# Kernel tuning notes

Measured on AMD Instinct MI355X. Metric: run time of the kernel, lower is better.

## Reference

```python
import jax, jax.numpy as jnp
import numpy as np

S, B, V, E, H = 64, 32, 32000, 512, 1024


def gru_cell(x, h, Wih, Whh, bih, bhh):
    # PyTorch GRU cell math. x: [B, in], h: [B, H]
    gi = x @ Wih.T + bih          # [B, 3H]
    gh = h @ Whh.T + bhh          # [B, 3H]
    ir, iz, inn = jnp.split(gi, 3, axis=-1)
    hr, hz, hn = jnp.split(gh, 3, axis=-1)
    r = jax.nn.sigmoid(ir + hr)
    z = jax.nn.sigmoid(iz + hz)
    n = jnp.tanh(inn + r * hn)
    return (1.0 - z) * n + z * h


def run_gru(xs, h0, Wih, Whh, bih, bhh):
    def step(h, x):
        h = gru_cell(x, h, Wih, Whh, bih, bhh)
        return h, h
    _, hs = jax.lax.scan(step, h0, xs)
    return hs  # [S, B, H]


def setup_inputs():
    key = jax.random.key(0)
    ks = jax.random.split(key, 24)
    n = lambda k, shp, s=0.05: (jax.random.normal(k, shp, jnp.float32) * s)
    inp = {
        "input_seq": jax.random.randint(ks[0], (S, B), 0, V),
        "target_seq": jax.random.randint(ks[1], (S, B), 0, V),
        "emb": n(ks[2], (V, E)),
        # bidirectional encoder GRU (forward / backward directions)
        "enc_Wih_f": n(ks[3], (3 * H, E)), "enc_Whh_f": n(ks[4], (3 * H, H)),
        "enc_bih_f": n(ks[5], (3 * H,)),  "enc_bhh_f": n(ks[6], (3 * H,)),
        "enc_Wih_b": n(ks[7], (3 * H, E)), "enc_Whh_b": n(ks[8], (3 * H, H)),
        "enc_bih_b": n(ks[9], (3 * H,)),  "enc_bhh_b": n(ks[10], (3 * H,)),
        "encoder_init": n(ks[11], (2, H), 0.1),
        # decoder GRU: input = token(E) + glimpse(2H) + last_output(E)
        "dec_Wih": n(ks[12], (3 * H, 2 * E + 2 * H)), "dec_Whh": n(ks[13], (3 * H, H)),
        "dec_bih": n(ks[14], (3 * H,)), "dec_bhh": n(ks[15], (3 * H,)),
        "dec_init_h": n(ks[16], (H,), 0.1),
        "dec_init_out": n(ks[17], (E,), 0.1),
        "attn_W1": n(ks[18], (H, 3 * H)),  # Linear(3H -> H, bias=False)
        "attn_W2": n(ks[19], (1, H)),      # Linear(H -> 1, bias=False)
        "out_W": n(ks[20], (V, H)), "out_b": n(ks[21], (V,)),
    }
    return inp


def reference(input_seq, target_seq, emb,
              enc_Wih_f, enc_Whh_f, enc_bih_f, enc_bhh_f,
              enc_Wih_b, enc_Whh_b, enc_bih_b, enc_bhh_b, encoder_init,
              dec_Wih, dec_Whh, dec_bih, dec_bhh, dec_init_h, dec_init_out,
              attn_W1, attn_W2, out_W, out_b):
    x = emb[input_seq]            # [S, B, E]
    tgt = emb[target_seq]         # [S, B, E]
    bsz = x.shape[1]

    # bidirectional encoder
    h0f = jnp.broadcast_to(encoder_init[0], (bsz, H))
    h0b = jnp.broadcast_to(encoder_init[1], (bsz, H))
    fwd = run_gru(x, h0f, enc_Wih_f, enc_Whh_f, enc_bih_f, enc_bhh_f)
    bwd = run_gru(x[::-1], h0b, enc_Wih_b, enc_Whh_b, enc_bih_b, enc_bhh_b)[::-1]
    enc = jnp.concatenate([fwd, bwd], axis=-1)  # [S, B, 2H]

    def step(carry, inp_t):
        h, last_out = carry                      # [B,H], [B,E]
        tok, tg = inp_t                          # [B,E], [B,E]
        hexp = jnp.broadcast_to(h[None], (S, bsz, H))
        a = jnp.concatenate([enc, hexp], axis=-1)            # [S, B, 3H]
        scores = jnp.tanh(a @ attn_W1.T) @ attn_W2.T          # [S, B, 1]
        # NOTE: original uses nn.Softmax(dim=1) on [S,B,1] -> softmax over BATCH dim
        w = jax.nn.softmax(scores, axis=1)
        glimpse = (enc * w).sum(axis=0)                       # [B, 2H]
        dec_in = jnp.concatenate([tok, glimpse, last_out], axis=-1)
        h = gru_cell(dec_in, h, dec_Wih, dec_Whh, dec_bih, dec_bhh)
        probs = jax.nn.softmax(h @ out_W.T + out_b, axis=1)   # [B, V]
        return (h, tg), probs

    h0 = jnp.broadcast_to(dec_init_h, (bsz, H))
    o0 = jnp.broadcast_to(dec_init_out, (bsz, E))
    _, outs = jax.lax.scan(step, (h0, o0), (x, tgt))
    return outs  # [S, B, V]
```

## Files before the change

kernel.cpp:

```cpp
#include <hip/hip_runtime.h>
#include <hip/hip_bf16.h>

#define S_ 64
#define B_ 32
#define V_ 32000
#define E_ 512
#define H_ 1024
#define H3_ 3072

typedef __hip_bfloat16 bf16;
typedef __attribute__((ext_vector_type(8))) short s8v;
typedef __attribute__((ext_vector_type(4))) float f4;
typedef unsigned long long ull;

__device__ __forceinline__ float b2f(bf16 x){ return __bfloat162float(x); }
__device__ __forceinline__ bf16  f2b(float x){ return __float2bfloat16(x); }
__device__ __forceinline__ float bfu2f(unsigned short u){
  union { unsigned u; float f; } c; c.u = ((unsigned)u) << 16; return c.f;
}
#define MFMA16(a,b,c) __builtin_amdgcn_mfma_f32_16x16x32_bf16((a),(b),(c),0,0,0)

__device__ __forceinline__ float fsigmoid(float x){ return 1.f/(1.f + __expf(-x)); }
__device__ __forceinline__ float ftanh(float x){ float e2 = __expf(2.f*x); return 1.f - 2.f/(e2 + 1.f); }

__device__ __forceinline__ void gl16(const bf16* g, bf16* l){
  __builtin_amdgcn_global_load_lds((const __attribute__((address_space(1))) void*)g,
                                   (__attribute__((address_space(3))) void*)l, 16, 0, 0);
}

__device__ __forceinline__ ull dld64(const void* p){
  return __hip_atomic_load((const ull*)p, __ATOMIC_RELAXED, __HIP_MEMORY_SCOPE_AGENT);
}
__device__ __forceinline__ void dst64(void* p, ull v){
  __hip_atomic_store((ull*)p, v, __ATOMIC_RELAXED, __HIP_MEMORY_SCOPE_AGENT);
}
__device__ __forceinline__ float dldf(const void* p){
  unsigned u = __hip_atomic_load((const unsigned*)p, __ATOMIC_RELAXED, __HIP_MEMORY_SCOPE_AGENT);
  union{unsigned u; float f;} c; c.u=u; return c.f;
}
__device__ __forceinline__ unsigned dldu(const unsigned* p){
  return __hip_atomic_load(p, __ATOMIC_RELAXED, __HIP_MEMORY_SCOPE_AGENT);
}
__device__ __forceinline__ void dstu(unsigned* p, unsigned v){
  __hip_atomic_store(p, v, __ATOMIC_RELAXED, __HIP_MEMORY_SCOPE_AGENT);
}

__device__ __forceinline__ void pbar(unsigned* bar, unsigned ep, int bid, int nblk){
  __syncthreads();
  if (bid == 0){
    const int i = threadIdx.x;
    if (i > 0 && i < nblk){
      while (dldu(bar + i*32) < ep) __builtin_amdgcn_s_sleep(1);
    }
    __syncthreads();
    if (i < nblk) dstu(bar + 4096 + i*32, ep);
  } else if (threadIdx.x == 0){
    dstu(bar + bid*32, ep);
    while (dldu(bar + 4096 + bid*32) < ep) __builtin_amdgcn_s_sleep(1);
  }
  __syncthreads();
  asm volatile("" ::: "memory");
}

__device__ __forceinline__ void cast8(const float* __restrict__ s, bf16* __restrict__ d, int i){
  f4 a = *((const f4*)s + (size_t)i*2);
  f4 b = *((const f4*)s + (size_t)i*2 + 1);
  union { s8v v; bf16 h[8]; } o;
  #pragma unroll
  for (int k=0;k<4;k++){ o.h[k]=f2b(a[k]); o.h[4+k]=f2b(b[k]); }
  *((s8v*)d + i) = o.v;
}

__global__ __launch_bounds__(256) void prep_all_k(
  const float* __restrict__ emb, const int* __restrict__ iseq, const int* __restrict__ tseq,
  const float* __restrict__ dino,
  const float* __restrict__ wihf, const float* __restrict__ wihb,
  const float* __restrict__ whhf, const float* __restrict__ whhb,
  const float* __restrict__ whhd, const float* __restrict__ w1,
  const float* __restrict__ wihd, const float* __restrict__ outw,
  const float* __restrict__ einit, const float* __restrict__ bihf,
  const float* __restrict__ bihb, const float* __restrict__ dinh,
  bf16* __restrict__ x_b, bf16* __restrict__ lo_b,
  bf16* __restrict__ wihf_b, bf16* __restrict__ wihb_b,
  bf16* __restrict__ whhf_b, bf16* __restrict__ whhb_b,
  bf16* __restrict__ whhd_b, bf16* __restrict__ w1_b,
  bf16* __restrict__ wihd_b, bf16* __restrict__ outw_b,
  bf16* __restrict__ henc_b, float* __restrict__ hfE, float* __restrict__ bias_fb)
{
  const int task = blockIdx.y;
  const int stride = gridDim.x*256;
  const int i00 = blockIdx.x*256 + threadIdx.x;
  if (task < 8){
    const float* s; bf16* d; int n8;
    switch(task){
      case 0: s=wihf; d=wihf_b; n8=196608; break;
      case 1: s=wihb; d=wihb_b; n8=196608; break;
      case 2: s=whhf; d=whhf_b; n8=393216; break;
      case 3: s=whhb; d=whhb_b; n8=393216; break;
      case 4: s=whhd; d=whhd_b; n8=393216; break;
      case 5: s=w1;   d=w1_b;   n8=393216; break;
      case 6: s=wihd; d=wihd_b; n8=1179648; break;
      default: s=outw; d=outw_b; n8=4096000; break;
    }
    for (int i = i00; i < n8; i += stride) cast8(s, d, i);
  } else if (task == 8 || task == 9){
    for (int i = i00; i < 131072; i += stride){
      int row = i>>6, e8 = i&63;
      const float* src; bf16* d;
      if (task == 8){ src = emb + (size_t)iseq[row]*E_; d = x_b; }
      else {
        int t = row>>5, b = row&31;
        src = (t == 0) ? dino : (emb + (size_t)tseq[(t-1)*B_ + b]*E_);
        d = lo_b;
      }
      f4 a = *((const f4*)src + e8*2);
      f4 b = *((const f4*)src + e8*2 + 1);
      union { s8v v; bf16 h[8]; } o;
      #pragma unroll
      for (int k=0;k<4;k++){ o.h[k]=f2b(a[k]); o.h[4+k]=f2b(b[k]); }
      *((s8v*)d + i) = o.v;
    }
  } else {
    for (int i = i00; i < 8192; i += stride){
      int base = i*8;
      int dir = base>>15, rem = base&32767, col = rem&1023;
      const float* sp = einit + dir*H_ + col;
      f4 a = *(const f4*)sp, b = *(const f4*)(sp+4);
      union { s8v v; bf16 h[8]; } o;
      #pragma unroll
      for (int k=0;k<4;k++){ o.h[k]=f2b(a[k]); o.h[4+k]=f2b(b[k]); }
      *(s8v*)(henc_b + dir*32768 + rem) = o.v;
      *(f4*)(hfE + dir*32768 + rem) = a;
      *(f4*)(hfE + dir*32768 + rem + 4) = b;
      if (i < 6144) bias_fb[i] = (i < 3072) ? bihf[i] : bihb[i-3072];
    }
  }
}

template<int WB16>
__global__ __launch_bounds__(256) void gemm_bt(const bf16* __restrict__ A, int lda,
                                               const bf16* __restrict__ B, int ldb,
                                               const float* __restrict__ bias,
                                               void* __restrict__ Cp, int ldc, int K)
{
  __shared__ bf16 a_sm[128][32];
  __shared__ bf16 b_sm[128][32];
  const int tid = threadIdx.x;
  const int m0 = blockIdx.y*128, n0 = blockIdx.x*128;
  const int w = tid>>6, l = tid&63;
  const int wm = w>>1, wn = w&1;
  f4 acc[4][4];
  #pragma unroll
  for (int i=0;i<4;i++)
    #pragma unroll
    for (int j=0;j<4;j++) acc[i][j] = (f4){0.f,0.f,0.f,0.f};
  const int ar = l&15, koff = (l>>4)*8;
  const int glr = l>>2, gls = (l&3)*8;
  for (int k0 = 0; k0 < K; k0 += 32){
    __syncthreads();
    #pragma unroll
    for (int o = 0; o < 2; ++o){
      const int oo = w*2 + o;
      gl16(A + (size_t)(m0 + oo*16 + glr)*lda + k0 + gls, &a_sm[oo*16][0]);
      gl16(B + (size_t)(n0 + oo*16 + glr)*ldb + k0 + gls, &b_sm[oo*16][0]);
    }
    __syncthreads();
    s8v av[4], bv[4];
    #pragma unroll
    for (int i=0;i<4;i++) av[i] = *(const s8v*)&a_sm[wm*64 + i*16 + ar][koff];
    #pragma unroll
    for (int j=0;j<4;j++) bv[j] = *(const s8v*)&b_sm[wn*64 + j*16 + ar][koff];
    #pragma unroll
    for (int i=0;i<4;i++)
      #pragma unroll
      for (int j=0;j<4;j++)
        acc[i][j] = MFMA16(av[i], bv[j], acc[i][j]);
  }
  const int rb = (l>>4)*4;
  #pragma unroll
  for (int i=0;i<4;i++){
    #pragma unroll
    for (int j=0;j<4;j++){
      int col = n0 + wn*64 + j*16 + ar;
      float badd = bias ? bias[col] : 0.f;
      #pragma unroll
      for (int r=0;r<4;r++){
        int row = m0 + wm*64 + i*16 + rb + r;
        size_t idx = (size_t)row*ldc + col;
        float v = acc[i][j][r] + badd;
        if (WB16) ((bf16*)Cp)[idx] = f2b(v);
        else      ((float*)Cp)[idx] = v;
      }
    }
  }
}

__global__ __launch_bounds__(256) void gemm_dual(const bf16* __restrict__ A1, const bf16* __restrict__ A2,
                                                 const bf16* __restrict__ Bw, const float* __restrict__ bias,
                                                 float* __restrict__ C)
{
  __shared__ bf16 a_sm[128][32];
  __shared__ bf16 b_sm[128][32];
  const int tid = threadIdx.x;
  const int m0 = blockIdx.y*128, n0 = blockIdx.x*128;
  const int w = tid>>6, l = tid&63;
  const int wm = w>>1, wn = w&1;
  f4 acc[4][4];
  #pragma unroll
  for (int i=0;i<4;i++)
    #pragma unroll
    for (int j=0;j<4;j++) acc[i][j] = (f4){0.f,0.f,0.f,0.f};
  const int ar = l&15, koff = (l>>4)*8;
  const int glr = l>>2, gls = (l&3)*8;
  #pragma unroll 1
  for (int p = 0; p < 2; ++p){
    const bf16* Ax = p ? A2 : A1;
    const int cb = p ? 2560 : 0;
    for (int k0 = 0; k0 < 512; k0 += 32){
      __syncthreads();
      #pragma unroll
      for (int o = 0; o < 2; ++o){
        const int oo = w*2 + o;
        gl16(Ax + (size_t)(m0 + oo*16 + glr)*512 + k0 + gls, &a_sm[oo*16][0]);
        gl16(Bw + (size_t)(n0 + oo*16 + glr)*3072 + cb + k0 + gls, &b_sm[oo*16][0]);
      }
      __syncthreads();
      s8v av[4], bv[4];
      #pragma unroll
      for (int i=0;i<4;i++) av[i] = *(const s8v*)&a_sm[wm*64 + i*16 + ar][koff];
      #pragma unroll
      for (int j=0;j<4;j++) bv[j] = *(const s8v*)&b_sm[wn*64 + j*16 + ar][koff];
      #pragma unroll
      for (int i=0;i<4;i++)
        #pragma unroll
        for (int j=0;j<4;j++)
          acc[i][j] = MFMA16(av[i], bv[j], acc[i][j]);
    }
  }
  const int rb = (l>>4)*4;
  #pragma unroll
  for (int i=0;i<4;i++){
    #pragma unroll
    for (int j=0;j<4;j++){
      int col = n0 + wn*64 + j*16 + ar;
      float badd = bias[col];
      #pragma unroll
      for (int r=0;r<4;r++){
        int row = m0 + wm*64 + i*16 + rb + r;
        C[(size_t)row*H3_ + col] = acc[i][j][r] + badd;
      }
    }
  }
}

__global__ __launch_bounds__(256) void out_gemm_k(
  const bf16* __restrict__ A, const bf16* __restrict__ Bw,
  const float* __restrict__ bias, bf16* __restrict__ C)
{
  __shared__ bf16 a_sm[128][32];
  __shared__ bf16 b_sm[128][32];
  const int tid = threadIdx.x;
  const int bid = blockIdx.x;
  const int xcd = bid & 7, kk = bid >> 3;
  const int super = kk >> 6, rem = kk & 63;
  const int sm = super & 1, sn = super >> 1;
  const int mi = rem & 7, nj = rem >> 3;
  const int mt = sm*8 + mi, nl = sn*8 + nj;
  const int nt = nl*8 + xcd;
  if (nt >= 250) return;
  const int m0 = mt*128, n0 = nt*128;
  const int w = tid>>6, l = tid&63;
  const int wm = w>>1, wn = w&1;
  f4 acc[4][4];
  #pragma unroll
  for (int i=0;i<4;i++)
    #pragma unroll
    for (int j=0;j<4;j++) acc[i][j] = (f4){0.f,0.f,0.f,0.f};
  const int ar = l&15, koff = (l>>4)*8;
  const int glr = l>>2, gls = (l&3)*8;
  for (int k0 = 0; k0 < 1024; k0 += 32){
    __syncthreads();
    #pragma unroll
    for (int o = 0; o < 2; ++o){
      const int oo = w*2 + o;
      gl16(A + (size_t)(m0 + oo*16 + glr)*1024 + k0 + gls, &a_sm[oo*16][0]);
      gl16(Bw + (size_t)(n0 + oo*16 + glr)*1024 + k0 + gls, &b_sm[oo*16][0]);
    }
    __syncthreads();
    s8v av[4], bv[4];
    #pragma unroll
    for (int i=0;i<4;i++) av[i] = *(const s8v*)&a_sm[wm*64 + i*16 + ar][koff];
    #pragma unroll
    for (int j=0;j<4;j++) bv[j] = *(const s8v*)&b_sm[wn*64 + j*16 + ar][koff];
    #pragma unroll
    for (int i=0;i<4;i++)
      #pragma unroll
      for (int j=0;j<4;j++)
        acc[i][j] = MFMA16(av[i], bv[j], acc[i][j]);
  }
  const int rb = (l>>4)*4;
  float bj[4];
  #pragma unroll
  for (int j=0;j<4;j++) bj[j] = bias[n0 + wn*64 + j*16 + ar];
  #pragma unroll
  for (int i=0;i<4;i++){
    #pragma unroll
    for (int j=0;j<4;j++){
      const int col = n0 + wn*64 + j*16 + ar;
      #pragma unroll
      for (int r=0;r<4;r++){
        const int row = m0 + wm*64 + i*16 + rb + r;
        C[(size_t)row*V_ + col] = f2b(acc[i][j][r] + bj[j]);
      }
    }
  }
}

__global__ __launch_bounds__(256) void logit_stats_k(const bf16* __restrict__ lg,
                                                     float* __restrict__ rowM, float* __restrict__ rowL){
  __shared__ float wm[4], wl[4];
  const int tid = threadIdx.x;
  const bf16* p = lg + (size_t)blockIdx.x*V_;
  float m = -1e30f, lsum = 0.f;
  for (int c = tid; c < V_/8; c += 256){
    union { s8v v; unsigned short us[8]; } u;
    u.v = *((const s8v*)p + c);
    #pragma unroll
    for (int k = 0; k < 8; ++k){
      float v = bfu2f(u.us[k]);
      float mn = fmaxf(m, v);
      lsum = lsum*__expf(m - mn) + __expf(v - mn);
      m = mn;
    }
  }
  #pragma unroll
  for (int o = 32; o; o >>= 1){
    float mo = __shfl_xor(m, o), lo_ = __shfl_xor(lsum, o);
    float mn = fmaxf(m, mo);
    lsum = lsum*__expf(m - mn) + lo_*__expf(mo - mn);
    m = mn;
  }
  if ((tid&63)==0){ wm[tid>>6] = m; wl[tid>>6] = lsum; }
  __syncthreads();
  if (tid == 0){
    float M = fmaxf(fmaxf(wm[0],wm[1]), fmaxf(wm[2],wm[3]));
    float L = wl[0]*__expf(wm[0]-M) + wl[1]*__expf(wm[1]-M)
            + wl[2]*__expf(wm[2]-M) + wl[3]*__expf(wm[3]-M);
    rowM[blockIdx.x] = M;
    rowL[blockIdx.x] = L;
  }
}

__global__ __launch_bounds__(256) void norm_k(const bf16* __restrict__ lg,
                                              const float* __restrict__ rowM, const float* __restrict__ rowL,
                                              float* __restrict__ out){
  const int tid = threadIdx.x;
  const int row = blockIdx.x;
  const float M = rowM[row], inv = 1.f/rowL[row];
  const bf16* p = lg + (size_t)row*V_;
  float* q = out + (size_t)row*V_;
  for (int c = tid; c < V_/8; c += 256){
    union { s8v v; unsigned short us[8]; } u;
    u.v = *((const s8v*)p + c);
    f4 o0, o1;
    #pragma unroll
    for (int k = 0; k < 4; ++k) o0[k] = __expf(bfu2f(u.us[k]) - M)*inv;
    #pragma unroll
    for (int k = 0; k < 4; ++k) o1[k] = __expf(bfu2f(u.us[4+k]) - M)*inv;
    *((f4*)q + c*2)     = o0;
    *((f4*)q + c*2 + 1) = o1;
  }
}

__global__ __launch_bounds__(256) void enc_step_k(
  const float* __restrict__ gi_fb,
  const bf16* __restrict__ whhf, const bf16* __restrict__ whhb,
  const float* __restrict__ bhhf, const float* __restrict__ bhhb,
  const bf16* __restrict__ hrd_base, bf16* __restrict__ hwr_base,
  float* __restrict__ hfE, bf16* __restrict__ enc_out, int s)
{
  __shared__ bf16 hst[16][1032];
  __shared__ bf16 hsT[16][64];
  const int tid = threadIdx.x, bid = blockIdx.x;
  const int w = tid>>6, l = tid&63;
  const int lr = l&15, koff = (l>>4)*8, rb = (l>>4)*4;
  const int x = bid&7, g3 = bid>>3;
  const int dir = x>>2;
  const int mt = g3>>2;
  const int jtb = (x&3)*16 + (g3&3)*4;
  const int jt = jtb + w;
  const int col = jt*16 + lr;
  const bf16* W    = dir ? whhb : whhf;
  const float* bhh = dir ? bhhb : bhhf;
  const float br_ = bhh[col], bz_ = bhh[H_+col], bn_ = bhh[2*H_+col];
  const bf16* pr = W + (size_t)(jt*16 + lr)*H_ + koff;
  const bf16* pz = pr + (size_t)H_*H_;
  const bf16* pn = pz + (size_t)H_*H_;
  {
    const bf16* src = hrd_base + dir*32768 + (size_t)mt*16*H_;
    #pragma unroll
    for (int c = 0; c < 8; ++c){
      int g = c*256 + tid;
      int row = g>>7, off = g&127;
      *(s8v*)&hst[row][off*8] = *(const s8v*)(src + (size_t)row*H_ + off*8);
    }
  }
  __syncthreads();
  f4 accr = (f4){0,0,0,0}, accz = (f4){0,0,0,0}, accn = (f4){0,0,0,0};
  #pragma unroll 4
  for (int k0 = 0; k0 < H_; k0 += 32){
    s8v a = *(const s8v*)&hst[lr][koff + k0];
    accr = MFMA16(a, *(const s8v*)(pr + k0), accr);
    accz = MFMA16(a, *(const s8v*)(pz + k0), accz);
    accn = MFMA16(a, *(const s8v*)(pn + k0), accn);
  }
  const int es = dir ? (63 - s) : s;
  const int dcol = dir*3072 + col;
  #pragma unroll
  for (int ri = 0; ri < 4; ++ri){
    const int b_ = mt*16 + rb + ri;
    const size_t gr = (size_t)(es*B_ + b_)*6144;
    float ir = gi_fb[gr + dcol], iz = gi_fb[gr + 1024 + dcol], inn = gi_fb[gr + 2048 + dcol];
    float rg = fsigmoid(ir + accr[ri] + br_);
    float zg = fsigmoid(iz + accz[ri] + bz_);
    float ng = ftanh(inn + rg*(accn[ri] + bn_));
    float hold = hfE[dir*32768 + b_*H_ + col];
    float hnew = (1.f - zg)*ng + zg*hold;
    hfE[dir*32768 + b_*H_ + col] = hnew;
    hsT[rb+ri][w*16+lr] = f2b(hnew);
  }
  __syncthreads();
  {
    const int row = tid>>4, seg = tid&15;
    ull v = *(ull*)&hsT[row][seg*4];
    *(ull*)(hwr_base + dir*32768 + (size_t)(mt*16+row)*H_ + jtb*16 + seg*4) = v;
    *(ull*)(enc_out + (size_t)(es*B_ + mt*16+row)*2048 + dir*H_ + jtb*16 + seg*4) = v;
  }
}

__global__ __launch_bounds__(256) void dec_persist_k(
  const float* __restrict__ gi_d,
  const bf16* __restrict__ encW1b,
  const bf16* __restrict__ encWgb,
  const bf16* __restrict__ whhd, const float* __restrict__ bhhd,
  const bf16* __restrict__ w1b,
  const float* __restrict__ attnW2,
  const float* __restrict__ dinh,
  bf16* __restrict__ hdb,
  bf16* __restrict__ hW1b,
  float* __restrict__ gh,
  float* __restrict__ wat,
  bf16* __restrict__ h_all,
  unsigned* __restrict__ bar)
{
  __shared__ bf16 hst[16][1032];
  __shared__ float ghT[16][128];
  __shared__ bf16 hwT[16][128];
  __shared__ float w2st[1024];
  __shared__ float scl[32];
  __shared__ float watv[32];
  __shared__ float watst[64];
  __shared__ float part_[4][3][256];
  __shared__ bf16 hnewst[256];
  const int tid = threadIdx.x, bid = blockIdx.x;
  const int w = tid>>6, l = tid&63;
  const int lr = l&15, koff = (l>>4)*8;
  const int x = bid&7, g3 = bid>>3;
  const int db = 4*x + (g3&3), jq = g3>>2;
  const int jD = jq*256 + tid;
  w2st[tid] = attnW2[tid];
  w2st[tid+256] = attnW2[tid+256];
  w2st[tid+512] = attnW2[tid+512];
  w2st[tid+768] = attnW2[tid+768];
  float hreg = dinh[jD];
  hnewst[tid] = f2b(hreg);
  __syncthreads();
  if (tid < 64) dst64(hdb + (size_t)db*H_ + jq*256 + tid*4, *(ull*)&hnewst[tid*4]);
  pbar(bar, 1u, bid, 128);
  unsigned ep = 2u;
  for (int t = 0; t < 64; ++t){
    if (bid < 64){
      const bool isP = bid < 16;
      const int hmt = isP ? (bid&1) : ((bid-16)&1);
      {
        const bf16* src = hdb + (size_t)hmt*16*H_;
        #pragma unroll
        for (int c = 0; c < 16; ++c){
          int g = c*256 + tid;
          *(ull*)&hst[g>>8][(g&255)*4] = dld64(src + g*4);
        }
      }
      __syncthreads();
      if (isP){
        const int x2 = bid>>1;
        const int pjt0 = x2*8 + w*2;
        #pragma unroll
        for (int q = 0; q < 2; ++q){
          const bf16* pb = w1b + (size_t)((pjt0+q)*16 + lr)*H3_ + 2048 + koff;
          f4 acc = (f4){0,0,0,0};
          #pragma unroll 4
          for (int k0 = 0; k0 < H_; k0 += 32)
            acc = MFMA16(*(const s8v*)&hst[lr][koff+k0], *(const s8v*)(pb+k0), acc);
          #pragma unroll
          for (int r = 0; r < 4; ++r)
            hwT[(l>>4)*4+r][(w*2+q)*16 + lr] = f2b(acc[r]);
        }
        __syncthreads();
        #pragma unroll
        for (int i = 0; i < 2; ++i){
          int idx = tid + i*256;
          int row = idx>>5, seg = idx&31;
          dst64(hW1b + (size_t)(hmt*16+row)*H_ + x2*128 + seg*4, *(ull*)&hwT[row][seg*4]);
        }
      } else {
        const int gb = bid - 16;
        const int rest = gb>>1;
        const int x3 = rest/3, gkk = rest%3;
        const int ntb = x3*24 + gkk*8;
        #pragma unroll
        for (int q = 0; q < 2; ++q){
          const int nt = ntb + w*2 + q;
          const bf16* pb = whhd + (size_t)(nt*16 + lr)*H_ + koff;
          const float bv = bhhd[nt*16 + lr];
          f4 acc = (f4){0,0,0,0};
          #pragma unroll 4
          for (int k0 = 0; k0 < H_; k0 += 32)
            acc = MFMA16(*(const s8v*)&hst[lr][koff+k0], *(const s8v*)(pb+k0), acc);
          #pragma unroll
          for (int r = 0; r < 4; ++r)
            ghT[(l>>4)*4+r][(w*2+q)*16 + lr] = acc[r] + bv;
        }
        __syncthreads();
        #pragma unroll
        for (int i = 0; i < 4; ++i){
          int idx = tid + i*256;
          int row = idx>>6, seg = idx&63;
          union{ float f[2]; ull u; } pk;
          pk.f[0] = ghT[row][seg*2]; pk.f[1] = ghT[row][seg*2+1];
          dst64(gh + (size_t)(hmt*16+row)*H3_ + ntb*16 + seg*2, pk.u);
        }
      }
    }
    pbar(bar, ep++, bid, 128);
    if (bid < 64){
      const int s = bid;
      const int b = tid>>3, part = tid&7;
      const bf16* hp = hW1b + (size_t)b*H_ + part*128;
      const bf16* epr = encW1b + ((size_t)s*B_ + b)*H_ + part*128;
      const float* wp = w2st + part*128;
      float p = 0.f;
      #pragma unroll 4
      for (int ii = 0; ii < 16; ++ii){
        union { ull u2[2]; unsigned short uu[8]; } hv;
        hv.u2[0] = dld64(hp + ii*8);
        hv.u2[1] = dld64(hp + ii*8 + 4);
        union { s8v v; unsigned short uu[8]; } ev;
        ev.v = *(const s8v*)(epr + ii*8);
        #pragma unroll
        for (int k = 0; k < 8; ++k){
          float xx = bfu2f(ev.uu[k]) + bfu2f(hv.uu[k]);
          p += wp[ii*8+k]*ftanh(xx);
        }
      }
      p += __shfl_xor(p,1); p += __shfl_xor(p,2); p += __shfl_xor(p,4);
      if (part == 0) scl[b] = p;
      __syncthreads();
      if (tid < 32){
        float v = scl[tid];
        float m = v;
        #pragma unroll
        for (int o = 1; o <= 16; o <<= 1) m = fmaxf(m, __shfl_xor(m, o));
        float e = __expf(v - m);
        float Z = e;
        #pragma unroll
        for (int o = 1; o <= 16; o <<= 1) Z += __shfl_xor(Z, o);
        watv[tid] = e/Z;
      }
      __syncthreads();
      if (tid < 16){
        union{ float f[2]; ull u; } pk;
        pk.f[0] = watv[tid*2]; pk.f[1] = watv[tid*2+1];
        dst64(wat + s*B_ + tid*2, pk.u);
      }
    }
    pbar(bar, ep++, bid, 128);
    {
      if (tid < 64) watst[tid] = dldf(wat + tid*B_ + db);
      float hr_ = dldf(gh + (size_t)db*H3_ + jD);
      float hz_ = dldf(gh + (size_t)db*H3_ + H_ + jD);
      float hn_ = dldf(gh + (size_t)db*H3_ + 2*H_ + jD);
      __syncthreads();
      const int lane = tid&63, wv = tid>>6;
      const int j0 = jq*256 + lane*4;
      f4 g0 = (f4){0,0,0,0}, g1 = (f4){0,0,0,0}, g2 = (f4){0,0,0,0};
      #pragma unroll 4
      for (int i = 0; i < 16; ++i){
        const int s2 = wv*16 + i;
        const float wt = watst[s2];
        const bf16* ro = encWgb + ((size_t)s2*B_ + db)*H3_;
        union{ ull u; unsigned short us[4]; } v0, v1, v2;
        v0.u = *(const ull*)(ro + j0);
        v1.u = *(const ull*)(ro + H_ + j0);
        v2.u = *(const ull*)(ro + 2*H_ + j0);
        #pragma unroll
        for (int k = 0; k < 4; ++k){
          g0[k] += wt*bfu2f(v0.us[k]);
          g1[k] += wt*bfu2f(v1.us[k]);
          g2[k] += wt*bfu2f(v2.us[k]);
        }
      }
      *(f4*)&part_[wv][0][lane*4] = g0;
      *(f4*)&part_[wv][1][lane*4] = g1;
      *(f4*)&part_[wv][2][lane*4] = g2;
      __syncthreads();
      float G0 = part_[0][0][tid]+part_[1][0][tid]+part_[2][0][tid]+part_[3][0][tid];
      float G1 = part_[0][1][tid]+part_[1][1][tid]+part_[2][1][tid]+part_[3][1][tid];
      float G2 = part_[0][2][tid]+part_[1][2][tid]+part_[2][2][tid]+part_[3][2][tid];
      const float* gp = gi_d + ((size_t)t*B_ + db)*H3_ + jD;
      float ir  = gp[0]    + G0;
      float iz  = gp[H_]   + G1;
      float inn = gp[2*H_] + G2;
      float rg = fsigmoid(ir + hr_);
      float zg = fsigmoid(iz + hz_);
      float ng = ftanh(inn + rg*hn_);
      float hnew = (1.f - zg)*ng + zg*hreg;
      hreg = hnew;
      hnewst[tid] = f2b(hnew);
      __syncthreads();
      if (tid < 64){
        ull v = *(ull*)&hnewst[tid*4];
        dst64(hdb + (size_t)db*H_ + jq*256 + tid*4, v);
        *(ull*)(h_all + ((size_t)t*B_ + db)*H_ + jq*256 + tid*4) = v;
      }
    }
    pbar(bar, ep++, bid, 128);
  }
}

extern "C" void kernel_launch(void* const* d_in, const int* in_sizes, int n_in,
                              void* d_out, int out_size, void* d_ws, size_t ws_size,
                              hipStream_t stream)
{
  (void)in_sizes; (void)n_in; (void)out_size; (void)ws_size;
  const int*   iseq  = (const int*)d_in[0];
  const int*   tseq  = (const int*)d_in[1];
  const float* emb   = (const float*)d_in[2];
  const float* wihf  = (const float*)d_in[3];
  const float* whhf_f= (const float*)d_in[4];
  const float* bihf  = (const float*)d_in[5];
  const float* bhhf  = (const float*)d_in[6];
  const float* wihb  = (const float*)d_in[7];
  const float* whhb_f= (const float*)d_in[8];
  const float* bihb  = (const float*)d_in[9];
  const float* bhhb  = (const float*)d_in[10];
  const float* einit = (const float*)d_in[11];
  const float* wihd  = (const float*)d_in[12];
  const float* whhd_f= (const float*)d_in[13];
  const float* bihd  = (const float*)d_in[14];
  const float* bhhd  = (const float*)d_in[15];
  const float* dinh  = (const float*)d_in[16];
  const float* dino  = (const float*)d_in[17];
  const float* w1    = (const float*)d_in[18];
  const float* w2    = (const float*)d_in[19];
  const float* outw  = (const float*)d_in[20];
  const float* outb  = (const float*)d_in[21];
  float* out = (float*)d_out;

  char* ws = (char*)d_ws;
  size_t off = 0;
  auto alloc = [&](size_t bytes)->char*{ char* p = ws + off; off += (bytes + 255) & ~(size_t)255; return p; };
  bf16* logits_b = (bf16*)ws;
  bf16* x_b      = (bf16*)alloc((size_t)2048*512*2);
  bf16* lo_b     = (bf16*)alloc((size_t)2048*512*2);
  bf16* wihf_b   = (bf16*)alloc((size_t)3072*512*2);
  bf16* wihb_b   = (bf16*)alloc((size_t)3072*512*2);
  bf16* whhf_b   = (bf16*)alloc((size_t)3072*1024*2);
  bf16* whhb_b   = (bf16*)alloc((size_t)3072*1024*2);
  bf16* wihd_b   = (bf16*)alloc((size_t)3072*3072*2);
  bf16* whhd_b   = (bf16*)alloc((size_t)3072*1024*2);
  bf16* w1_b     = (bf16*)alloc((size_t)1024*3072*2);
  float* gi_fb   = (float*)alloc((size_t)2048*6144*4);
  float* gi_d    = (float*)alloc((size_t)2048*3072*4);
  bf16* enc_b    = (bf16*)alloc((size_t)2048*2048*2);
  bf16* encW1_b  = (bf16*)alloc((size_t)2048*1024*2);
  bf16* encWg_b  = (bf16*)alloc((size_t)2048*3072*2);
  float* bias_fb = (float*)alloc((size_t)6144*4);
  bf16*  henc_b  = (bf16*)alloc((size_t)2*65536*2);
  float* hfE     = (float*)alloc((size_t)2*32768*4);
  bf16*  hdb     = (bf16*)alloc((size_t)32768*2);
  bf16*  hW1b    = (bf16*)alloc((size_t)32768*2);
  float* ghb     = (float*)alloc((size_t)32*3072*4);
  float* wat     = (float*)alloc((size_t)64*32*4);
  unsigned* bar  = (unsigned*)alloc((size_t)32768);
  float* rowM    = (float*)alloc((size_t)2048*4);
  float* rowL    = (float*)alloc((size_t)2048*4);
  bf16* outw_b   = (bf16*)alloc((size_t)32000*1024*2);
  bf16*  hall_b  = (bf16*)alloc((size_t)2048*1024*2);

  hipMemsetAsync(bar, 0, 32768, stream);

  prep_all_k<<<dim3(512,11), 256, 0, stream>>>(
      emb, iseq, tseq, dino,
      wihf, wihb, whhf_f, whhb_f, whhd_f, w1, wihd, outw,
      einit, bihf, bihb, dinh,
      x_b, lo_b, wihf_b, wihb_b, whhf_b, whhb_b, whhd_b, w1_b, wihd_b, outw_b,
      henc_b, hfE, bias_fb);

  gemm_bt<0><<<dim3(48,16), 256, 0, stream>>>(x_b, 512, wihf_b, 512, bias_fb, gi_fb, 6144, 512);
  gemm_dual<<<dim3(24,16), 256, 0, stream>>>(x_b, lo_b, wihd_b, bihd, gi_d);

  for (int s = 0; s < 64; ++s){
    const bf16* hrd = henc_b + (size_t)(s&1)*65536;
    bf16*       hwr = henc_b + (size_t)((s+1)&1)*65536;
    enc_step_k<<<64, 256, 0, stream>>>(gi_fb, whhf_b, whhb_b, bhhf, bhhb,
                                       hrd, hwr, hfE, enc_b, s);
  }

  gemm_bt<1><<<dim3(8,16),  256, 0, stream>>>(enc_b, 2048, w1_b,       3072, nullptr, encW1_b, 1024, 2048);
  gemm_bt<1><<<dim3(24,16), 256, 0, stream>>>(enc_b, 2048, wihd_b+512, 3072, nullptr, encWg_b, 3072, 2048);

  dec_persist_k<<<128, 256, 0, stream>>>(gi_d, encW1_b, encWg_b, whhd_b, bhhd, w1_b, w2, dinh,
                                         hdb, hW1b, ghb, wat, hall_b, bar);

  out_gemm_k<<<4096, 256, 0, stream>>>(hall_b, outw_b, outb, logits_b);
  logit_stats_k<<<2048, 256, 0, stream>>>(logits_b, rowM, rowL);
  norm_k<<<2048, 256, 0, stream>>>(logits_b, rowM, rowL, out);
}
```

Measured before the change: 3.343 ms.

## Split decoder phases across disjoint block groups and widen glimpse loads

```diff
diff --git a/kernel.cpp b/kernel.cpp
--- a/kernel.cpp
+++ b/kernel.cpp
@@ -453,20 +453,29 @@
   bf16* __restrict__ h_all,
   unsigned* __restrict__ bar)
 {
-  __shared__ bf16 hst[16][1032];
+  __shared__ union {
+    bf16 hst[16][1032];
+    float part8[8][3][256];
+  } u;
   __shared__ float ghT[16][128];
   __shared__ bf16 hwT[16][128];
   __shared__ float w2st[1024];
   __shared__ float scl[32];
   __shared__ float watv[32];
   __shared__ float watst[64];
-  __shared__ float part_[4][3][256];
   __shared__ bf16 hnewst[256];
   const int tid = threadIdx.x, bid = blockIdx.x;
   const int w = tid>>6, l = tid&63;
   const int lr = l&15, koff = (l>>4)*8;
-  const int x = bid&7, g3 = bid>>3;
-  const int db = 4*x + (g3&3), jq = g3>>2;
+  const int xcd = bid&7;
+  const bool isP = bid < 16;
+  const bool isG = (bid >= 16) && (bid < 64);
+  const bool isS = bid >= 64;
+  const int grank = (bid-16)>>3;
+  const int gcol = grank>>1;
+  const int ntb = xcd*24 + gcol*8;
+  const int sS = xcd*8 + ((bid-64)>>3);
+  const int db = 4*xcd + ((bid>>3)&3), jq = bid>>5;
   const int jD = jq*256 + tid;
   w2st[tid] = attnW2[tid];
   w2st[tid+256] = attnW2[tid+256];
@@ -479,20 +488,19 @@
   pbar(bar, 1u, bid, 128);
   unsigned ep = 2u;
   for (int t = 0; t < 64; ++t){
-    if (bid < 64){
-      const bool isP = bid < 16;
-      const int hmt = isP ? (bid&1) : ((bid-16)&1);
+    if (isP || isG){
+      const int hmt = isP ? (bid>>3) : (grank&1);
       {
         const bf16* src = hdb + (size_t)hmt*16*H_;
         #pragma unroll
         for (int c = 0; c < 16; ++c){
           int g = c*256 + tid;
-          *(ull*)&hst[g>>8][(g&255)*4] = dld64(src + g*4);
+          *(ull*)&u.hst[g>>8][(g&255)*4] = dld64(src + g*4);
         }
       }
       __syncthreads();
       if (isP){
-        const int x2 = bid>>1;
+        const int x2 = xcd;
         const int pjt0 = x2*8 + w*2;
         #pragma unroll
         for (int q = 0; q < 2; ++q){
@@ -500,7 +508,7 @@
           f4 acc = (f4){0,0,0,0};
           #pragma unroll 4
           for (int k0 = 0; k0 < H_; k0 += 32)
-            acc = MFMA16(*(const s8v*)&hst[lr][koff+k0], *(const s8v*)(pb+k0), acc);
+            acc = MFMA16(*(const s8v*)&u.hst[lr][koff+k0], *(const s8v*)(pb+k0), acc);
           #pragma unroll
           for (int r = 0; r < 4; ++r)
             hwT[(l>>4)*4+r][(w*2+q)*16 + lr] = f2b(acc[r]);
@@ -513,10 +521,6 @@
           dst64(hW1b + (size_t)(hmt*16+row)*H_ + x2*128 + seg*4, *(ull*)&hwT[row][seg*4]);
         }
       } else {
-        const int gb = bid - 16;
-        const int rest = gb>>1;
-        const int x3 = rest/3, gkk = rest%3;
-        const int ntb = x3*24 + gkk*8;
         #pragma unroll
         for (int q = 0; q < 2; ++q){
           const int nt = ntb + w*2 + q;
@@ -525,28 +529,28 @@
           f4 acc = (f4){0,0,0,0};
           #pragma unroll 4
           for (int k0 = 0; k0 < H_; k0 += 32)
-            acc = MFMA16(*(const s8v*)&hst[lr][koff+k0], *(const s8v*)(pb+k0), acc);
+            acc = MFMA16(*(const s8v*)&u.hst[lr][koff+k0], *(const s8v*)(pb+k0), acc);
           #pragma unroll
           for (int r = 0; r < 4; ++r)
             ghT[(l>>4)*4+r][(w*2+q)*16 + lr] = acc[r] + bv;
         }
         __syncthreads();
+        const int hmt2 = grank&1;
         #pragma unroll
         for (int i = 0; i < 4; ++i){
           int idx = tid + i*256;
           int row = idx>>6, seg = idx&63;
-          union{ float f[2]; ull u; } pk;
+          union{ float f[2]; ull uu; } pk;
           pk.f[0] = ghT[row][seg*2]; pk.f[1] = ghT[row][seg*2+1];
-          dst64(gh + (size_t)(hmt*16+row)*H3_ + ntb*16 + seg*2, pk.u);
+          dst64(gh + (size_t)(hmt2*16+row)*H3_ + ntb*16 + seg*2, pk.uu);
         }
       }
     }
     pbar(bar, ep++, bid, 128);
-    if (bid < 64){
-      const int s = bid;
+    if (isS){
       const int b = tid>>3, part = tid&7;
       const bf16* hp = hW1b + (size_t)b*H_ + part*128;
-      const bf16* epr = encW1b + ((size_t)s*B_ + b)*H_ + part*128;
+      const bf16* epr = encW1b + ((size_t)sS*B_ + b)*H_ + part*128;
       const float* wp = w2st + part*128;
       float p = 0.f;
       #pragma unroll 4
@@ -578,9 +582,9 @@
       }
       __syncthreads();
       if (tid < 16){
-        union{ float f[2]; ull u; } pk;
+        union{ float f[2]; ull uu; } pk;
         pk.f[0] = watv[tid*2]; pk.f[1] = watv[tid*2+1];
-        dst64(wat + s*B_ + tid*2, pk.u);
+        dst64(wat + sS*B_ + tid*2, pk.uu);
       }
     }
     pbar(bar, ep++, bid, 128);
@@ -590,32 +594,41 @@
       float hz_ = dldf(gh + (size_t)db*H3_ + H_ + jD);
       float hn_ = dldf(gh + (size_t)db*H3_ + 2*H_ + jD);
       __syncthreads();
-      const int lane = tid&63, wv = tid>>6;
-      const int j0 = jq*256 + lane*4;
-      f4 g0 = (f4){0,0,0,0}, g1 = (f4){0,0,0,0}, g2 = (f4){0,0,0,0};
-      #pragma unroll 4
-      for (int i = 0; i < 16; ++i){
-        const int s2 = wv*16 + i;
+      const int hl = l&31, sh = l>>5;
+      const int wv = tid>>6;
+      const int j0 = jq*256 + hl*8;
+      f4 a0lo = (f4){0,0,0,0}, a0hi = (f4){0,0,0,0};
+      f4 a1lo = (f4){0,0,0,0}, a1hi = (f4){0,0,0,0};
+      f4 a2lo = (f4){0,0,0,0}, a2hi = (f4){0,0,0,0};
+      #pragma unroll 2
+      for (int i = 0; i < 8; ++i){
+        const int s2 = wv*16 + sh*8 + i;
         const float wt = watst[s2];
-        const bf16* ro = encWgb + ((size_t)s2*B_ + db)*H3_;
-        union{ ull u; unsigned short us[4]; } v0, v1, v2;
-        v0.u = *(const ull*)(ro + j0);
-        v1.u = *(const ull*)(ro + H_ + j0);
-        v2.u = *(const ull*)(ro + 2*H_ + j0);
+        const bf16* ro = encWgb + ((size_t)s2*B_ + db)*H3_ + j0;
+        union{ s8v v; unsigned short us[8]; } v0, v1, v2;
+        v0.v = *(const s8v*)(ro);
+        v1.v = *(const s8v*)(ro + H_);
+        v2.v = *(const s8v*)(ro + 2*H_);
         #pragma unroll
         for (int k = 0; k < 4; ++k){
-          g0[k] += wt*bfu2f(v0.us[k]);
-          g1[k] += wt*bfu2f(v1.us[k]);
-          g2[k] += wt*bfu2f(v2.us[k]);
+          a0lo[k] += wt*bfu2f(v0.us[k]);   a0hi[k] += wt*bfu2f(v0.us[4+k]);
+          a1lo[k] += wt*bfu2f(v1.us[k]);   a1hi[k] += wt*bfu2f(v1.us[4+k]);
+          a2lo[k] += wt*bfu2f(v2.us[k]);   a2hi[k] += wt*bfu2f(v2.us[4+k]);
         }
       }
-      *(f4*)&part_[wv][0][lane*4] = g0;
-      *(f4*)&part_[wv][1][lane*4] = g1;
-      *(f4*)&part_[wv][2][lane*4] = g2;
-      __syncthreads();
-      float G0 = part_[0][0][tid]+part_[1][0][tid]+part_[2][0][tid]+part_[3][0][tid];
-      float G1 = part_[0][1][tid]+part_[1][1][tid]+part_[2][1][tid]+part_[3][1][tid];
-      float G2 = part_[0][2][tid]+part_[1][2][tid]+part_[2][2][tid]+part_[3][2][tid];
+      __syncthreads();
+      const int hw = wv*2 + sh;
+      *(f4*)&u.part8[hw][0][hl*8]   = a0lo;  *(f4*)&u.part8[hw][0][hl*8+4] = a0hi;
+      *(f4*)&u.part8[hw][1][hl*8]   = a1lo;  *(f4*)&u.part8[hw][1][hl*8+4] = a1hi;
+      *(f4*)&u.part8[hw][2][hl*8]   = a2lo;  *(f4*)&u.part8[hw][2][hl*8+4] = a2hi;
+      __syncthreads();
+      float G0 = 0.f, G1 = 0.f, G2 = 0.f;
+      #pragma unroll
+      for (int h8 = 0; h8 < 8; ++h8){
+        G0 += u.part8[h8][0][tid];
+        G1 += u.part8[h8][1][tid];
+        G2 += u.part8[h8][2][tid];
+      }
       const float* gp = gi_d + ((size_t)t*B_ + db)*H3_ + jD;
       float ir  = gp[0]    + G0;
       float iz  = gp[H_]   + G1;
```

Result: slower. 3.659 ms (+9.5%).
